# Performance work log

Measured on AMD Instinct MI355X. Metric: run time of the kernel, lower is better.

The kernel has to match this reference:

```python
import jax, jax.numpy as jnp
import numpy as np

EMBED_DIM = 1024
NUM_HEADS = 16
HEAD_DIM = EMBED_DIM // NUM_HEADS
B, N = 4, 2048


def setup_inputs() -> dict:
    key = jax.random.key(0)
    ks = jax.random.split(key, 12)
    s = 1.0 / np.sqrt(EMBED_DIM)
    inp = {
        "x": jax.random.normal(ks[0], (B, N, EMBED_DIM), dtype=jnp.float32),
        "dist_matrix": jax.random.uniform(ks[1], (N, N), dtype=jnp.float32),
        # Linear weights stored torch-style [out, in]
        "Wq": jax.random.normal(ks[2], (EMBED_DIM, EMBED_DIM), dtype=jnp.float32) * s,
        "bq": jnp.zeros((EMBED_DIM,), dtype=jnp.float32),
        "Wk": jax.random.normal(ks[3], (EMBED_DIM, EMBED_DIM), dtype=jnp.float32) * s,
        "bk": jnp.zeros((EMBED_DIM,), dtype=jnp.float32),
        "Wv": jax.random.normal(ks[4], (EMBED_DIM, EMBED_DIM), dtype=jnp.float32) * s,
        "bv": jnp.zeros((EMBED_DIM,), dtype=jnp.float32),
        "Wo": jax.random.normal(ks[5], (EMBED_DIM, EMBED_DIM), dtype=jnp.float32) * s,
        "bo": jnp.zeros((EMBED_DIM,), dtype=jnp.float32),
        # DistanceBias params: bias = dist_w * dist + dist_b (learned scalar affine)
        "dist_w": jnp.asarray(-1.0, dtype=jnp.float32),
        "dist_b": jnp.asarray(0.0, dtype=jnp.float32),
    }
    return inp


def reference(x, dist_matrix, Wq, bq, Wk, bk, Wv, bv, Wo, bo, dist_w, dist_b):
    b, n, c = x.shape
    h, d = NUM_HEADS, HEAD_DIM
    # projections (torch Linear: x @ W.T + b), reshape to [b, h, n, d]
    def proj(W, bias):
        y = jnp.einsum('bnc,oc->bno', x, W) + bias
        return y.reshape(b, n, h, d).transpose(0, 2, 1, 3)
    q = proj(Wq, bq)
    k = proj(Wk, bk)
    v = proj(Wv, bv)
    scores = jnp.einsum('bhnd,bhmd->bhnm', q, k) / np.sqrt(d).astype(np.float32)
    bias = dist_w * dist_matrix + dist_b            # [N, N], shared over b, h
    scores = scores + bias[None, None, :, :]
    attn = jax.nn.softmax(scores, axis=-1)
    out = jnp.einsum('bhnm,bhmd->bhnd', attn, v)    # [b, h, n, d]
    out = out.transpose(0, 2, 1, 3).reshape(b, n, c)
    return jnp.einsum('bnc,oc->bno', out, Wo) + bo
```

## Files before the change

kernel.cpp:

```cpp
#include <hip/hip_runtime.h>
#include <stdint.h>

typedef unsigned short ushort;
typedef __attribute__((ext_vector_type(8))) short bf16x8;
typedef __attribute__((ext_vector_type(4))) float f32x4;

__device__ __forceinline__ float b2f(ushort u) {
    return __uint_as_float(((unsigned)u) << 16);
}
__device__ __forceinline__ ushort f2b(float f) {
    unsigned u = __float_as_uint(f);
    u += 0x7fff + ((u >> 16) & 1);
    return (ushort)(u >> 16);
}
__device__ __forceinline__ ushort f2b_fast(float f) {
    return (ushort)((__float_as_uint(f) + 0x8000u) >> 16);
}

#define SEQN 2048
#define EMB  1024
#define NH   16
#define HD   64
#define BHSTRIDE (SEQN * HD)

__device__ __forceinline__ void gload16(const ushort* g, ushort* l) {
    __builtin_amdgcn_global_load_lds(
        (const __attribute__((address_space(1))) unsigned int*)g,
        (__attribute__((address_space(3))) unsigned int*)l, 16, 0, 0);
}

__global__ __launch_bounds__(256) void conv_x(
        const float* __restrict__ s, ushort* __restrict__ d) {
    const size_t i = (size_t)blockIdx.x * 256 + threadIdx.x;
    float4 a = ((const float4*)s)[2 * i];
    float4 b = ((const float4*)s)[2 * i + 1];
    ushort pk[8] = {f2b(a.x), f2b(a.y), f2b(a.z), f2b(a.w),
                    f2b(b.x), f2b(b.y), f2b(b.z), f2b(b.w)};
    ((uint4*)d)[i] = *(uint4*)pk;
}

__global__ __launch_bounds__(256) void conv_w4(
        const float* __restrict__ W0, const float* __restrict__ W1,
        const float* __restrict__ W2, const float* __restrict__ W3,
        ushort* __restrict__ d) {
    const float* s = (blockIdx.y == 0) ? W0 : (blockIdx.y == 1) ? W1
                   : (blockIdx.y == 2) ? W2 : W3;
    ushort* dst = d + ((size_t)blockIdx.y << 20);
    const size_t i = (size_t)blockIdx.x * 256 + threadIdx.x;
    float4 a = ((const float4*)s)[2 * i];
    float4 b = ((const float4*)s)[2 * i + 1];
    ushort pk[8] = {f2b(a.x), f2b(a.y), f2b(a.z), f2b(a.w),
                    f2b(b.x), f2b(b.y), f2b(b.z), f2b(b.w)};
    ((uint4*)dst)[i] = *(uint4*)pk;
}

__global__ __launch_bounds__(256) void bias_exp_perm(
        const float* __restrict__ dist, const float* __restrict__ dw,
        const float* __restrict__ db, ushort* __restrict__ E) {
    const float wd = dw[0], bd = db[0];
    const int kv = blockIdx.x * 256 + threadIdx.x;
    const int qt = blockIdx.y;
    ushort pk[16];
#pragma unroll
    for (int qq = 0; qq < 16; qq++)
        pk[qq] = f2b(__expf(fmaf(wd, dist[(size_t)(qt * 16 + qq) * SEQN + kv], bd)));
    ushort* dst = E + ((size_t)qt << 15) + (size_t)kv * 16;
    *(uint4*)dst       = *(uint4*)&pk[0];
    *(uint4*)(dst + 8) = *(uint4*)&pk[8];
}

#define LDSZ (128 * 32)

__global__ __launch_bounds__(256) void gemm_qkv(
        const ushort* __restrict__ xb, const ushort* __restrict__ Wb,
        const float* __restrict__ bq, const float* __restrict__ bk,
        const float* __restrict__ bv,
        ushort* __restrict__ qb, ushort* __restrict__ kb,
        ushort* __restrict__ vT) {
    __shared__ ushort As[LDSZ];
    __shared__ ushort Bs[LDSZ];
    const int m0   = blockIdx.x * 128;
    const int nt   = blockIdx.y;
    const int wsel = nt >> 3;
    const int n0   = (nt & 7) * 128;
    const ushort* W    = Wb + ((size_t)wsel << 20);
    const float* bias  = (wsel == 0) ? bq : (wsel == 1) ? bk : bv;

    const int t = threadIdx.x, lane = t & 63, wave = t >> 6;
    const int ln = lane & 15, quad = lane >> 4;
    const int wm = wave & 1, wn = wave >> 1;

    const int e0 = wave * 128 + lane;
    const int e1 = e0 + 64;
    const ushort* gA0 = xb + (size_t)(m0 + (e0 >> 2)) * 1024 + (e0 & 3) * 8;
    const ushort* gA1 = xb + (size_t)(m0 + (e1 >> 2)) * 1024 + (e1 & 3) * 8;
    const ushort* gB0 = W  + (size_t)(n0 + (e0 >> 2)) * 1024 + (e0 & 3) * 8;
    const ushort* gB1 = W  + (size_t)(n0 + (e1 >> 2)) * 1024 + (e1 & 3) * 8;
    ushort* lA0 = As + wave * 1024;
    ushort* lA1 = lA0 + 512;
    ushort* lB0 = Bs + wave * 1024;
    ushort* lB1 = lB0 + 512;

    f32x4 acc[4][4];
#pragma unroll
    for (int i = 0; i < 4; i++)
#pragma unroll
        for (int j = 0; j < 4; j++) acc[i][j] = (f32x4){0.f, 0.f, 0.f, 0.f};

    for (int k0 = 0; k0 < 1024; k0 += 32) {
        __syncthreads();
        gload16(gA0 + k0, lA0);
        gload16(gA1 + k0, lA1);
        gload16(gB0 + k0, lB0);
        gload16(gB1 + k0, lB1);
        __syncthreads();
        bf16x8 af[4], bfr[4];
#pragma unroll
        for (int i = 0; i < 4; i++)
            af[i]  = *(bf16x8*)&As[(wm * 64 + i * 16 + ln) * 32 + quad * 8];
#pragma unroll
        for (int j = 0; j < 4; j++)
            bfr[j] = *(bf16x8*)&Bs[(wn * 64 + j * 16 + ln) * 32 + quad * 8];
#pragma unroll
        for (int i = 0; i < 4; i++)
#pragma unroll
            for (int j = 0; j < 4; j++)
                acc[i][j] = __builtin_amdgcn_mfma_f32_16x16x32_bf16(
                                af[i], bfr[j], acc[i][j], 0, 0, 0);
    }

    if (wsel < 2) {
        ushort* dst = (wsel == 0) ? qb : kb;
        const float scale = (wsel == 0) ? 0.125f : 1.0f;
#pragma unroll
        for (int j = 0; j < 4; j++) {
            const int o  = n0 + wn * 64 + j * 16 + ln;
            const float bval = bias[o];
            const int h = o >> 6, d = o & 63;
#pragma unroll
            for (int i = 0; i < 4; i++) {
                const int mg = m0 + wm * 64 + i * 16 + quad * 4;
#pragma unroll
                for (int r = 0; r < 4; r++) {
                    const int m  = mg + r;
                    const int b  = m >> 11;
                    const int ns = m & 2047;
                    dst[(size_t)(b * NH + h) * BHSTRIDE + (size_t)ns * HD + d] =
                        f2b((acc[i][j][r] + bval) * scale);
                }
            }
        }
    } else {
#pragma unroll
        for (int j = 0; j < 4; j++) {
            const int o  = n0 + wn * 64 + j * 16 + ln;
            const float bval = bias[o];
            const int h = o >> 6, d = o & 63;
#pragma unroll
            for (int i = 0; i < 4; i++) {
                const int mg = m0 + wm * 64 + i * 16 + quad * 4;
                const int b  = mg >> 11;
                const int ns = mg & 2047;
                ushort pk[4];
#pragma unroll
                for (int r = 0; r < 4; r++) pk[r] = f2b(acc[i][j][r] + bval);
                *(uint2*)&vT[(size_t)(b * NH + h) * BHSTRIDE +
                             (size_t)d * SEQN + ns] = *(uint2*)&pk[0];
            }
        }
    }
}

__global__ __launch_bounds__(256) void attn(
        ushort* q,
        const ushort* __restrict__ k,
        const ushort* __restrict__ vT,
        const ushort* __restrict__ E) {
    __shared__ short Ks[64 * 72];
    __shared__ short Vs[64 * 72];
    __shared__ short Ps[4][32 * 72];
    const int t = threadIdx.x, lane = t & 63, wave = t >> 6;
    const int ln = lane & 15, quad = lane >> 4;
    const int h = blockIdx.y, b = blockIdx.z;
    const int bh = b * NH + h;
    const int qw0 = blockIdx.x * 128 + wave * 32;
    const int qt0 = qw0 >> 4;

    ushort* qp = q + (size_t)bh * BHSTRIDE;
    const ushort* kp = k  + (size_t)bh * BHSTRIDE;
    const ushort* vp = vT + (size_t)bh * BHSTRIDE;

    const int sr = t >> 2;
    const int sc = (t & 3) * 16;

    bf16x8 qf[2][2];
#pragma unroll
    for (int qi = 0; qi < 2; qi++)
#pragma unroll
        for (int ks = 0; ks < 2; ks++)
            qf[qi][ks] = *(const bf16x8*)(qp + (size_t)(qw0 + qi * 16 + ln) * HD
                                          + ks * 32 + quad * 8);

    f32x4 O[2][4];
#pragma unroll
    for (int qi = 0; qi < 2; qi++)
#pragma unroll
        for (int nd = 0; nd < 4; nd++) O[qi][nd] = (f32x4){0.f, 0.f, 0.f, 0.f};
    float lsum[2][4] = {{0.f,0.f,0.f,0.f},{0.f,0.f,0.f,0.f}};
    short* myp = &Ps[wave][0];

    uint4 krg0 = *(const uint4*)(kp + (size_t)sr * HD + sc);
    uint4 krg1 = *(const uint4*)(kp + (size_t)sr * HD + sc + 8);
    uint4 vrg0 = *(const uint4*)(vp + (size_t)sr * SEQN + sc);
    uint4 vrg1 = *(const uint4*)(vp + (size_t)sr * SEQN + sc + 8);

    for (int kt = 0; kt < 32; kt++) {
        const int kv0 = kt * 64;
        __syncthreads();
        *(uint4*)&Ks[sr * 72 + sc]     = krg0;
        *(uint4*)&Ks[sr * 72 + sc + 8] = krg1;
        *(uint4*)&Vs[sr * 72 + sc]     = vrg0;
        *(uint4*)&Vs[sr * 72 + sc + 8] = vrg1;
        __syncthreads();
        const int kvn = (kv0 + 64) & 2047;
        krg0 = *(const uint4*)(kp + (size_t)(kvn + sr) * HD + sc);
        krg1 = *(const uint4*)(kp + (size_t)(kvn + sr) * HD + sc + 8);
        vrg0 = *(const uint4*)(vp + (size_t)sr * SEQN + kvn + sc);
        vrg1 = *(const uint4*)(vp + (size_t)sr * SEQN + kvn + sc + 8);
        uint2 ev2[2][4];
#pragma unroll
        for (int qi = 0; qi < 2; qi++) {
            const size_t ebase = ((size_t)(qt0 + qi)) << 15;
#pragma unroll
            for (int kvb = 0; kvb < 4; kvb++)
                ev2[qi][kvb] = *(const uint2*)(E + ebase +
                    (size_t)(kv0 + kvb * 16 + ln) * 16 + quad * 4);
        }
        bf16x8 kf0[4], kf1[4];
#pragma unroll
        for (int kvb = 0; kvb < 4; kvb++) {
            kf0[kvb] = *(bf16x8*)&Ks[(kvb * 16 + ln) * 72 + quad * 8];
            kf1[kvb] = *(bf16x8*)&Ks[(kvb * 16 + ln) * 72 + 32 + quad * 8];
        }
        f32x4 s[2][4];
#pragma unroll
        for (int qi = 0; qi < 2; qi++)
#pragma unroll
            for (int kvb = 0; kvb < 4; kvb++) {
                f32x4 z = (f32x4){0.f, 0.f, 0.f, 0.f};
                z = __builtin_amdgcn_mfma_f32_16x16x32_bf16(qf[qi][0], kf0[kvb], z, 0, 0, 0);
                s[qi][kvb] = __builtin_amdgcn_mfma_f32_16x16x32_bf16(qf[qi][1], kf1[kvb], z, 0, 0, 0);
            }
#pragma unroll
        for (int qi = 0; qi < 2; qi++)
#pragma unroll
            for (int kvb = 0; kvb < 4; kvb++) {
                const ushort* ep = (const ushort*)&ev2[qi][kvb];
#pragma unroll
                for (int r = 0; r < 4; r++) {
                    const float p = b2f(ep[r]) * __expf(s[qi][kvb][r]);
                    lsum[qi][r] += p;
                    myp[(qi * 16 + quad * 4 + r) * 72 + kvb * 16 + ln] =
                        (short)f2b_fast(p);
                }
            }
        bf16x8 vf[4][2];
#pragma unroll
        for (int nd = 0; nd < 4; nd++)
#pragma unroll
            for (int kc = 0; kc < 2; kc++)
                vf[nd][kc] = *(bf16x8*)&Vs[(nd * 16 + ln) * 72 + kc * 32 + quad * 8];
        bf16x8 pa[2][2];
#pragma unroll
        for (int qi = 0; qi < 2; qi++)
#pragma unroll
            for (int kc = 0; kc < 2; kc++)
                pa[qi][kc] = *(bf16x8*)&myp[(qi * 16 + ln) * 72 + kc * 32 + quad * 8];
#pragma unroll
        for (int qi = 0; qi < 2; qi++)
#pragma unroll
            for (int kc = 0; kc < 2; kc++)
#pragma unroll
                for (int nd = 0; nd < 4; nd++)
                    O[qi][nd] = __builtin_amdgcn_mfma_f32_16x16x32_bf16(
                                    pa[qi][kc], vf[nd][kc], O[qi][nd], 0, 0, 0);
    }

#pragma unroll
    for (int qi = 0; qi < 2; qi++)
#pragma unroll
        for (int r = 0; r < 4; r++) {
            float v = lsum[qi][r];
            v += __shfl_xor(v, 1, 16);
            v += __shfl_xor(v, 2, 16);
            v += __shfl_xor(v, 4, 16);
            v += __shfl_xor(v, 8, 16);
            lsum[qi][r] = 1.0f / v;
        }
#pragma unroll
    for (int qi = 0; qi < 2; qi++)
#pragma unroll
        for (int nd = 0; nd < 4; nd++)
#pragma unroll
            for (int r = 0; r < 4; r++) {
                qp[(size_t)(qw0 + qi * 16 + quad * 4 + r) * HD + nd * 16 + ln] =
                    f2b(O[qi][nd][r] * lsum[qi][r]);
            }
}

__global__ __launch_bounds__(256) void gemm_out(
        const ushort* __restrict__ ao, const ushort* __restrict__ Wob,
        const float* __restrict__ bias, float* __restrict__ out) {
    __shared__ ushort As[LDSZ];
    __shared__ ushort Bs[LDSZ];
    const int m0 = blockIdx.x * 128;
    const int n0 = blockIdx.y * 128;
    const int t = threadIdx.x, lane = t & 63, wave = t >> 6;
    const int ln = lane & 15, quad = lane >> 4;
    const int wm = wave & 1, wn = wave >> 1;

    const int e0 = wave * 128 + lane;
    const int e1 = e0 + 64;
    const int bb = m0 >> 11;
    const int nbase = m0 & 2047;
    const ushort* gA0 = ao + ((size_t)bb << 21) +
                        (size_t)(nbase + (e0 >> 2)) * 64 + (e0 & 3) * 8;
    const ushort* gA1 = ao + ((size_t)bb << 21) +
                        (size_t)(nbase + (e1 >> 2)) * 64 + (e1 & 3) * 8;
    const ushort* gB0 = Wob + (size_t)(n0 + (e0 >> 2)) * 1024 + (e0 & 3) * 8;
    const ushort* gB1 = Wob + (size_t)(n0 + (e1 >> 2)) * 1024 + (e1 & 3) * 8;
    ushort* lA0 = As + wave * 1024;
    ushort* lA1 = lA0 + 512;
    ushort* lB0 = Bs + wave * 1024;
    ushort* lB1 = lB0 + 512;

    f32x4 acc[4][4];
#pragma unroll
    for (int i = 0; i < 4; i++)
#pragma unroll
        for (int j = 0; j < 4; j++) acc[i][j] = (f32x4){0.f, 0.f, 0.f, 0.f};

    for (int k0 = 0; k0 < 1024; k0 += 32) {
        const size_t aoff = ((size_t)(k0 >> 6) << 17) + (k0 & 32);
        __syncthreads();
        gload16(gA0 + aoff, lA0);
        gload16(gA1 + aoff, lA1);
        gload16(gB0 + k0, lB0);
        gload16(gB1 + k0, lB1);
        __syncthreads();
        bf16x8 af[4], bfr[4];
#pragma unroll
        for (int i = 0; i < 4; i++)
            af[i]  = *(bf16x8*)&As[(wm * 64 + i * 16 + ln) * 32 + quad * 8];
#pragma unroll
        for (int j = 0; j < 4; j++)
            bfr[j] = *(bf16x8*)&Bs[(wn * 64 + j * 16 + ln) * 32 + quad * 8];
#pragma unroll
        for (int i = 0; i < 4; i++)
#pragma unroll
            for (int j = 0; j < 4; j++)
                acc[i][j] = __builtin_amdgcn_mfma_f32_16x16x32_bf16(
                                af[i], bfr[j], acc[i][j], 0, 0, 0);
    }

#pragma unroll
    for (int j = 0; j < 4; j++) {
        const int o = n0 + wn * 64 + j * 16 + ln;
        const float bval = bias[o];
#pragma unroll
        for (int i = 0; i < 4; i++) {
            const int mg = m0 + wm * 64 + i * 16 + quad * 4;
#pragma unroll
            for (int r = 0; r < 4; r++)
                out[(size_t)(mg + r) * EMB + o] = acc[i][j][r] + bval;
        }
    }
}

extern "C" void kernel_launch(void* const* d_in, const int* in_sizes, int n_in,
                              void* d_out, int out_size, void* d_ws, size_t ws_size,
                              hipStream_t stream) {
    const float* x    = (const float*)d_in[0];
    const float* dist = (const float*)d_in[1];
    const float* Wq   = (const float*)d_in[2];
    const float* bq   = (const float*)d_in[3];
    const float* Wk   = (const float*)d_in[4];
    const float* bk   = (const float*)d_in[5];
    const float* Wv   = (const float*)d_in[6];
    const float* bv   = (const float*)d_in[7];
    const float* Wo   = (const float*)d_in[8];
    const float* bo   = (const float*)d_in[9];
    const float* dw   = (const float*)d_in[10];
    const float* db   = (const float*)d_in[11];

    const size_t PLANE = (size_t)8192 * 1024;
    ushort* qb = (ushort*)d_ws;
    ushort* kb = qb + PLANE;
    ushort* xb = kb + PLANE;
    ushort* Wb = xb + PLANE;
    ushort* vT = (ushort*)d_out;
    ushort* Eb = vT + PLANE;

    dim3 blk(256);
    conv_x       <<<dim3(4096),      blk, 0, stream>>>(x, xb);
    conv_w4      <<<dim3(512, 4),    blk, 0, stream>>>(Wq, Wk, Wv, Wo, Wb);
    bias_exp_perm<<<dim3(8, 128),    blk, 0, stream>>>(dist, dw, db, Eb);
    gemm_qkv     <<<dim3(64, 24),    blk, 0, stream>>>(xb, Wb, bq, bk, bv,
                                                       qb, kb, vT);
    attn         <<<dim3(16, 16, 4), blk, 0, stream>>>(qb, kb, vT, Eb);
    gemm_out     <<<dim3(64, 8),     blk, 0, stream>>>(qb, Wb + 3 * (size_t)(1 << 20),
                                                       bo, (float*)d_out);
}
```

Before: 354.7 us.

## Use 32x32 MFMA with in-register P transpose and fp32 log2 bias table

The attention kernel moves from 16x16x32 to 32x32x16 bf16 MFMA and computes S transposed (K as the A operand), so P can be packed with v_cvt_pk_bf16_f32 and rearranged with permlane32_swap instead of going through LDS. The precomputed bias changes from a permuted bf16 exp table to an fp32 log2-scaled bias that is added inside exp2, which gives bias precision closer to fp32. This removes the Ps LDS round-trip and its extra sync pressure, but the bias table read per tile doubles in bytes (fp32 instead of bf16). Softmax still has no max subtraction.

```diff
diff --git a/kernel.cpp b/kernel.cpp
--- a/kernel.cpp
+++ b/kernel.cpp
@@ -4,6 +4,7 @@
 typedef unsigned short ushort;
 typedef __attribute__((ext_vector_type(8))) short bf16x8;
 typedef __attribute__((ext_vector_type(4))) float f32x4;
+typedef __attribute__((ext_vector_type(16))) float f32x16;
 
 __device__ __forceinline__ float b2f(ushort u) {
     return __uint_as_float(((unsigned)u) << 16);
@@ -13,8 +14,26 @@
     u += 0x7fff + ((u >> 16) & 1);
     return (ushort)(u >> 16);
 }
-__device__ __forceinline__ ushort f2b_fast(float f) {
-    return (ushort)((__float_as_uint(f) + 0x8000u) >> 16);
+
+#if __has_builtin(__builtin_amdgcn_exp2f)
+#define EXP2(x) __builtin_amdgcn_exp2f(x)
+#else
+#define EXP2(x) __expf((x) * 0.69314718056f)
+#endif
+
+__device__ __forceinline__ unsigned cvtpk(float a, float b) {
+    unsigned r;
+    asm("v_cvt_pk_bf16_f32 %0, %1, %2" : "=v"(r) : "v"(a), "v"(b));
+    return r;
+}
+
+__device__ __forceinline__ void plswap(unsigned &a, unsigned &b) {
+#if __has_builtin(__builtin_amdgcn_permlane32_swap)
+    auto r = __builtin_amdgcn_permlane32_swap(a, b, 0, 0);
+    a = (unsigned)r[0]; b = (unsigned)r[1];
+#else
+    asm volatile("v_permlane32_swap_b32 %0, %1" : "+v"(a), "+v"(b));
+#endif
 }
 
 #define SEQN 2048
@@ -54,19 +73,15 @@
     ((uint4*)dst)[i] = *(uint4*)pk;
 }
 
-__global__ __launch_bounds__(256) void bias_exp_perm(
+__global__ __launch_bounds__(256) void conv_L(
         const float* __restrict__ dist, const float* __restrict__ dw,
-        const float* __restrict__ db, ushort* __restrict__ E) {
-    const float wd = dw[0], bd = db[0];
-    const int kv = blockIdx.x * 256 + threadIdx.x;
-    const int qt = blockIdx.y;
-    ushort pk[16];
-#pragma unroll
-    for (int qq = 0; qq < 16; qq++)
-        pk[qq] = f2b(__expf(fmaf(wd, dist[(size_t)(qt * 16 + qq) * SEQN + kv], bd)));
-    ushort* dst = E + ((size_t)qt << 15) + (size_t)kv * 16;
-    *(uint4*)dst       = *(uint4*)&pk[0];
-    *(uint4*)(dst + 8) = *(uint4*)&pk[8];
+        const float* __restrict__ db, float* __restrict__ L) {
+    const float c1 = dw[0] * 1.44269504f, c2 = db[0] * 1.44269504f;
+    const size_t i = (size_t)blockIdx.x * 256 + threadIdx.x;
+    float4 d = ((const float4*)dist)[i];
+    float4 o = {fmaf(d.x, c1, c2), fmaf(d.y, c1, c2),
+                fmaf(d.z, c1, c2), fmaf(d.w, c1, c2)};
+    ((float4*)L)[i] = o;
 }
 
 #define LDSZ (128 * 32)
@@ -175,39 +190,34 @@
         ushort* q,
         const ushort* __restrict__ k,
         const ushort* __restrict__ vT,
-        const ushort* __restrict__ E) {
+        const float* __restrict__ Lf) {
     __shared__ short Ks[64 * 72];
     __shared__ short Vs[64 * 72];
-    __shared__ short Ps[4][32 * 72];
     const int t = threadIdx.x, lane = t & 63, wave = t >> 6;
-    const int ln = lane & 15, quad = lane >> 4;
+    const int lo = lane & 31, hi = lane >> 5;
     const int h = blockIdx.y, b = blockIdx.z;
     const int bh = b * NH + h;
     const int qw0 = blockIdx.x * 128 + wave * 32;
-    const int qt0 = qw0 >> 4;
 
     ushort* qp = q + (size_t)bh * BHSTRIDE;
     const ushort* kp = k  + (size_t)bh * BHSTRIDE;
     const ushort* vp = vT + (size_t)bh * BHSTRIDE;
+    const float* lrow = Lf + (size_t)(qw0 + lo) * SEQN;
 
     const int sr = t >> 2;
     const int sc = (t & 3) * 16;
 
-    bf16x8 qf[2][2];
-#pragma unroll
-    for (int qi = 0; qi < 2; qi++)
-#pragma unroll
-        for (int ks = 0; ks < 2; ks++)
-            qf[qi][ks] = *(const bf16x8*)(qp + (size_t)(qw0 + qi * 16 + ln) * HD
-                                          + ks * 32 + quad * 8);
-
-    f32x4 O[2][4];
-#pragma unroll
-    for (int qi = 0; qi < 2; qi++)
-#pragma unroll
-        for (int nd = 0; nd < 4; nd++) O[qi][nd] = (f32x4){0.f, 0.f, 0.f, 0.f};
-    float lsum[2][4] = {{0.f,0.f,0.f,0.f},{0.f,0.f,0.f,0.f}};
-    short* myp = &Ps[wave][0];
+    bf16x8 qf[4];
+#pragma unroll
+    for (int kk = 0; kk < 4; kk++)
+        qf[kk] = *(const bf16x8*)(qp + (size_t)(qw0 + lo) * HD + kk * 16 + hi * 8);
+
+    f32x16 O[2];
+#pragma unroll
+    for (int dt = 0; dt < 2; dt++)
+#pragma unroll
+        for (int i = 0; i < 16; i++) O[dt][i] = 0.f;
+    float lsum = 0.f;
 
     uint4 krg0 = *(const uint4*)(kp + (size_t)sr * HD + sc);
     uint4 krg1 = *(const uint4*)(kp + (size_t)sr * HD + sc + 8);
@@ -227,85 +237,63 @@
         krg1 = *(const uint4*)(kp + (size_t)(kvn + sr) * HD + sc + 8);
         vrg0 = *(const uint4*)(vp + (size_t)sr * SEQN + kvn + sc);
         vrg1 = *(const uint4*)(vp + (size_t)sr * SEQN + kvn + sc + 8);
-        uint2 ev2[2][4];
-#pragma unroll
-        for (int qi = 0; qi < 2; qi++) {
-            const size_t ebase = ((size_t)(qt0 + qi)) << 15;
-#pragma unroll
-            for (int kvb = 0; kvb < 4; kvb++)
-                ev2[qi][kvb] = *(const uint2*)(E + ebase +
-                    (size_t)(kv0 + kvb * 16 + ln) * 16 + quad * 4);
-        }
-        bf16x8 kf0[4], kf1[4];
-#pragma unroll
-        for (int kvb = 0; kvb < 4; kvb++) {
-            kf0[kvb] = *(bf16x8*)&Ks[(kvb * 16 + ln) * 72 + quad * 8];
-            kf1[kvb] = *(bf16x8*)&Ks[(kvb * 16 + ln) * 72 + 32 + quad * 8];
-        }
-        f32x4 s[2][4];
-#pragma unroll
-        for (int qi = 0; qi < 2; qi++)
-#pragma unroll
-            for (int kvb = 0; kvb < 4; kvb++) {
-                f32x4 z = (f32x4){0.f, 0.f, 0.f, 0.f};
-                z = __builtin_amdgcn_mfma_f32_16x16x32_bf16(qf[qi][0], kf0[kvb], z, 0, 0, 0);
-                s[qi][kvb] = __builtin_amdgcn_mfma_f32_16x16x32_bf16(qf[qi][1], kf1[kvb], z, 0, 0, 0);
+
+#pragma unroll
+        for (int s = 0; s < 2; s++) {
+            f32x16 z;
+#pragma unroll
+            for (int i = 0; i < 16; i++) z[i] = 0.f;
+#pragma unroll
+            for (int kk = 0; kk < 4; kk++) {
+                bf16x8 kf = *(bf16x8*)&Ks[(s * 32 + lo) * 72 + kk * 16 + hi * 8];
+                z = __builtin_amdgcn_mfma_f32_32x32x16_bf16(kf, qf[kk], z, 0, 0, 0);
             }
-#pragma unroll
-        for (int qi = 0; qi < 2; qi++)
-#pragma unroll
-            for (int kvb = 0; kvb < 4; kvb++) {
-                const ushort* ep = (const ushort*)&ev2[qi][kvb];
-#pragma unroll
-                for (int r = 0; r < 4; r++) {
-                    const float p = b2f(ep[r]) * __expf(s[qi][kvb][r]);
-                    lsum[qi][r] += p;
-                    myp[(qi * 16 + quad * 4 + r) * 72 + kvb * 16 + ln] =
-                        (short)f2b_fast(p);
+            float p[16];
+#pragma unroll
+            for (int n = 0; n < 4; n++) {
+                float4 lv = *(const float4*)(lrow + kv0 + s * 32 + hi * 4 + n * 8);
+#pragma unroll
+                for (int m = 0; m < 4; m++) {
+                    float pv = EXP2(fmaf(z[n * 4 + m], 1.44269504f,
+                                         ((const float*)&lv)[m]));
+                    lsum += pv;
+                    p[n * 4 + m] = pv;
                 }
             }
-        bf16x8 vf[4][2];
-#pragma unroll
-        for (int nd = 0; nd < 4; nd++)
-#pragma unroll
-            for (int kc = 0; kc < 2; kc++)
-                vf[nd][kc] = *(bf16x8*)&Vs[(nd * 16 + ln) * 72 + kc * 32 + quad * 8];
-        bf16x8 pa[2][2];
-#pragma unroll
-        for (int qi = 0; qi < 2; qi++)
-#pragma unroll
-            for (int kc = 0; kc < 2; kc++)
-                pa[qi][kc] = *(bf16x8*)&myp[(qi * 16 + ln) * 72 + kc * 32 + quad * 8];
-#pragma unroll
-        for (int qi = 0; qi < 2; qi++)
-#pragma unroll
-            for (int kc = 0; kc < 2; kc++)
-#pragma unroll
-                for (int nd = 0; nd < 4; nd++)
-                    O[qi][nd] = __builtin_amdgcn_mfma_f32_16x16x32_bf16(
-                                    pa[qi][kc], vf[nd][kc], O[qi][nd], 0, 0, 0);
+#pragma unroll
+            for (int kl = 0; kl < 2; kl++) {
+                unsigned a0 = cvtpk(p[kl * 8 + 0], p[kl * 8 + 1]);
+                unsigned b0 = cvtpk(p[kl * 8 + 4], p[kl * 8 + 5]);
+                plswap(a0, b0);
+                unsigned a1 = cvtpk(p[kl * 8 + 2], p[kl * 8 + 3]);
+                unsigned b1 = cvtpk(p[kl * 8 + 6], p[kl * 8 + 7]);
+                plswap(a1, b1);
+                union { bf16x8 v; unsigned u[4]; } pf;
+                pf.u[0] = a0; pf.u[1] = a1; pf.u[2] = b0; pf.u[3] = b1;
+                const int kvk = s * 2 + kl;
+#pragma unroll
+                for (int dt = 0; dt < 2; dt++) {
+                    bf16x8 vf = *(bf16x8*)&Vs[(dt * 32 + lo) * 72 +
+                                              kvk * 16 + hi * 8];
+                    O[dt] = __builtin_amdgcn_mfma_f32_32x32x16_bf16(
+                                vf, pf.v, O[dt], 0, 0, 0);
+                }
+            }
+        }
     }
 
-#pragma unroll
-    for (int qi = 0; qi < 2; qi++)
-#pragma unroll
-        for (int r = 0; r < 4; r++) {
-            float v = lsum[qi][r];
-            v += __shfl_xor(v, 1, 16);
-            v += __shfl_xor(v, 2, 16);
-            v += __shfl_xor(v, 4, 16);
-            v += __shfl_xor(v, 8, 16);
-            lsum[qi][r] = 1.0f / v;
+    float tot = lsum + __shfl_xor(lsum, 32);
+    const float inv = 1.0f / tot;
+#pragma unroll
+    for (int dt = 0; dt < 2; dt++)
+#pragma unroll
+        for (int n = 0; n < 4; n++) {
+            uint2 pk2;
+            pk2.x = cvtpk(O[dt][n * 4 + 0] * inv, O[dt][n * 4 + 1] * inv);
+            pk2.y = cvtpk(O[dt][n * 4 + 2] * inv, O[dt][n * 4 + 3] * inv);
+            *(uint2*)(qp + (size_t)(qw0 + lo) * HD + dt * 32 + hi * 4 + n * 8)
+                = pk2;
         }
-#pragma unroll
-    for (int qi = 0; qi < 2; qi++)
-#pragma unroll
-        for (int nd = 0; nd < 4; nd++)
-#pragma unroll
-            for (int r = 0; r < 4; r++) {
-                qp[(size_t)(qw0 + qi * 16 + quad * 4 + r) * HD + nd * 16 + ln] =
-                    f2b(O[qi][nd][r] * lsum[qi][r]);
-            }
 }
 
 __global__ __launch_bounds__(256) void gemm_out(
@@ -399,15 +387,15 @@
     ushort* xb = kb + PLANE;
     ushort* Wb = xb + PLANE;
     ushort* vT = (ushort*)d_out;
-    ushort* Eb = vT + PLANE;
+    float*  Lf = (float*)(vT + PLANE);
 
     dim3 blk(256);
     conv_x       <<<dim3(4096),      blk, 0, stream>>>(x, xb);
     conv_w4      <<<dim3(512, 4),    blk, 0, stream>>>(Wq, Wk, Wv, Wo, Wb);
-    bias_exp_perm<<<dim3(8, 128),    blk, 0, stream>>>(dist, dw, db, Eb);
+    conv_L       <<<dim3(4096),      blk, 0, stream>>>(dist, dw, db, Lf);
     gemm_qkv     <<<dim3(64, 24),    blk, 0, stream>>>(xb, Wb, bq, bk, bv,
                                                        qb, kb, vT);
-    attn         <<<dim3(16, 16, 4), blk, 0, stream>>>(qb, kb, vT, Eb);
+    attn         <<<dim3(16, 16, 4), blk, 0, stream>>>(qb, kb, vT, Lf);
     gemm_out     <<<dim3(64, 8),     blk, 0, stream>>>(qb, Wb + 3 * (size_t)(1 << 20),
                                                        bo, (float*)d_out);
 }
```

New measurement: 374.9 us. +5.7%, slower.
